# Kernel tuning notes

Hardware: AMD Instinct MI355X
Metric: run time of the kernel (lower is better)

The kernel has to match this reference:

```python
import jax, jax.numpy as jnp
import numpy as np

IMAGE_W, IMAGE_H = 1024, 800
STRIDES = (8, 16, 32, 64, 128)
LEVEL_HW = ((100, 128), (50, 64), (25, 32), (13, 16), (7, 8))
TOP_N = 1000
MIN_SCORE = 0.01
NMS_THR = 0.6
MAX_DET = 100
NUM_CLASSES = 80
BATCH = 16


def _grid(h, w, stride, b):
    ys = (jnp.arange(h, dtype=jnp.float32) + 0.5) * stride
    xs = (jnp.arange(w, dtype=jnp.float32) + 0.5) * stride
    gx, gy = jnp.meshgrid(xs, ys)  # [h, w]
    pos = jnp.stack([gx, gy], axis=-1)  # [h, w, 2] = (x, y)
    return jnp.broadcast_to(pos, (b, h, w, 2))


def setup_inputs() -> dict:
    key = jax.random.key(0)
    inp = {}
    for i, ((h, w), s) in enumerate(zip(LEVEL_HW, STRIDES)):
        key, k1, k2, k3 = jax.random.split(key, 4)
        inp[f"cls{i}"] = jax.random.normal(k1, (BATCH, h, w, NUM_CLASSES), jnp.float32)
        # +3 so exp(reg) gives realistic ~20px box extents
        inp[f"reg{i}"] = jax.random.normal(k2, (BATCH, h, w, 4), jnp.float32) + 3.0
        inp[f"ctr{i}"] = jax.random.normal(k3, (BATCH, h, w, 1), jnp.float32)
        inp[f"pos{i}"] = _grid(h, w, s, BATCH)
    return inp


def _level_filter(cls, reg, ctr, pos):
    b = cls.shape[0]
    cls = jax.nn.sigmoid(cls).reshape(b, -1, NUM_CLASSES)
    reg = jnp.exp(reg).reshape(b, -1, 4)
    ctr = jax.nn.sigmoid(ctr).reshape(b, -1)
    pos = pos.reshape(b, -1, 2)
    scores = jnp.sqrt(jnp.max(cls, axis=2) * ctr)  # [b, n]
    classes = jnp.argmax(cls, axis=2)  # [b, n] int
    if scores.shape[1] >= TOP_N:
        scores, idx = jax.lax.top_k(scores, TOP_N)
        classes = jnp.take_along_axis(classes, idx, axis=1)
        reg = jnp.take_along_axis(reg, idx[..., None], axis=1)
        pos = jnp.take_along_axis(pos, idx[..., None], axis=1)
        cls = jnp.take_along_axis(cls, idx[..., None], axis=1)
    return scores, classes, reg, pos, cls


def _decode_boxes(reg, pos):
    # ltrb offsets -> x1y1x2y2, truncate to int (torch .int()), clamp to image
    xy_min = pos - reg[..., 0:2]
    xy_max = pos + reg[..., 2:4]
    bx = jnp.trunc(jnp.concatenate([xy_min, xy_max], axis=-1))
    x1 = jnp.maximum(bx[..., 0], 0.0)
    y1 = jnp.maximum(bx[..., 1], 0.0)
    x2 = jnp.minimum(bx[..., 2], IMAGE_W - 1.0)
    y2 = jnp.minimum(bx[..., 3], IMAGE_H - 1.0)
    return jnp.stack([x1, y1, x2, y2], axis=-1)


def _nms_image(scores, classes, boxes, clsp):
    valid = scores > MIN_SCORE
    order = jnp.argsort(jnp.where(valid, -scores, jnp.inf))  # valid, desc score first
    s = scores[order]
    c = classes[order].astype(jnp.float32)
    b = boxes[order]
    cp = clsp[order]
    v = valid[order]
    # pairwise IoU (keep/suppress decisions are not differentiated)
    bb = jax.lax.stop_gradient(b)
    area = (bb[:, 2] - bb[:, 0]) * (bb[:, 3] - bb[:, 1])
    lt = jnp.maximum(bb[:, None, :2], bb[None, :, :2])
    rb = jnp.minimum(bb[:, None, 2:], bb[None, :, 2:])
    wh = jnp.maximum(rb - lt, 0.0)
    inter = wh[..., 0] * wh[..., 1]
    iou = inter / (area[:, None] + area[None, :] - inter)
    n = s.shape[0]
    idxs = jnp.arange(n)

    def body(i, keep):
        sup = keep[i] & (iou[i] > NMS_THR) & (idxs > i)
        return keep & ~sup

    keep = jax.lax.fori_loop(0, n, body, v)
    rank = jnp.cumsum(keep) - 1
    slot = jnp.where(keep & (rank < MAX_DET), rank, MAX_DET)  # MAX_DET -> dropped
    out_s = jnp.full((MAX_DET,), -1.0, jnp.float32).at[slot].set(s, mode="drop")
    out_c = jnp.full((MAX_DET,), -1.0, jnp.float32).at[slot].set(c, mode="drop")
    out_b = jnp.full((MAX_DET, 4), -1.0, jnp.float32).at[slot].set(b, mode="drop")
    out_cp = jnp.full((MAX_DET, NUM_CLASSES), -1.0, jnp.float32).at[slot].set(cp, mode="drop")
    return out_s, out_c, out_b, out_cp


def reference(cls0, cls1, cls2, cls3, cls4, reg0, reg1, reg2, reg3, reg4,
              ctr0, ctr1, ctr2, ctr3, ctr4, pos0, pos1, pos2, pos3, pos4):
    clss = [cls0, cls1, cls2, cls3, cls4]
    regs = [reg0, reg1, reg2, reg3, reg4]
    ctrs = [ctr0, ctr1, ctr2, ctr3, ctr4]
    poss = [pos0, pos1, pos2, pos3, pos4]
    parts = [_level_filter(c, r, t, p) for c, r, t, p in zip(clss, regs, ctrs, poss)]
    scores = jnp.concatenate([p[0] for p in parts], axis=1)
    classes = jnp.concatenate([p[1] for p in parts], axis=1)
    reg = jnp.concatenate([p[2] for p in parts], axis=1)
    pos = jnp.concatenate([p[3] for p in parts], axis=1)
    clsp = jnp.concatenate([p[4] for p in parts], axis=1)
    boxes = _decode_boxes(reg, pos)
    return jax.vmap(_nms_image)(scores, classes, boxes, clsp)
```

## Files before the change

kernel.cpp:

```cpp
#include <hip/hip_runtime.h>
#include <math.h>

#define TOTAL_G 17064
#define BATCHN  16
#define ALLF    0xFFFFFFFFFFFFFFFFull
#define INVALID_HI 0xC3DC28F5u

typedef unsigned long long u64;
typedef unsigned int u32;
typedef unsigned short u16;

#define KEYS0_OFF   0
#define KEYS1_OFF   1638400
#define KEYS234_OFF 2048000
#define CLSI_OFF    2187264
#define NC_OFF      2733312
#define T01_OFF     2733568
#define T512_OFF    2733824
#define CK_OFF      2733952
#define K512_OFF    3127168
#define KR_OFF      3192704
#define MSK_OFF     3258240
#define FB_OFF      3782528
#define SLOTK_OFF   4568960

struct Ptrs {
  const float *cls0,*cls1,*cls2,*cls3,*cls4;
  const float *reg0,*reg1,*reg2,*reg3,*reg4;
  const float *ctr0,*ctr1,*ctr2,*ctr3,*ctr4;
  const float *pos0,*pos1,*pos2,*pos3,*pos4;
  char *ws;
};

__device__ __forceinline__ float sigd(float x) {
  return (float)(1.0 / (1.0 + exp(-(double)x)));
}
__device__ __forceinline__ float dexp(float x) {
  return (float)exp((double)x);
}
__device__ __forceinline__ void levinfo(int gid, int& lev, int& idx, int& nl) {
  if      (gid < 12800) { lev=0; idx=gid;        nl=12800; }
  else if (gid < 16000) { lev=1; idx=gid-12800;  nl=3200;  }
  else if (gid < 16800) { lev=2; idx=gid-16000;  nl=800;   }
  else if (gid < 17008) { lev=3; idx=gid-16800;  nl=208;   }
  else                  { lev=4; idx=gid-17008;  nl=56;    }
}

__device__ __forceinline__ u64* ckeys_of(char* ws, int b) {
  return (u64*)(ws + CK_OFF + (size_t)b * 24576);
}
__device__ __forceinline__ u64* key512_of(char* ws, int b) {
  return (u64*)(ws + K512_OFF + (size_t)b * 4096);
}
__device__ __forceinline__ u64* krank_of(char* ws, int b) {
  return (u64*)(ws + KR_OFF + (size_t)b * 4096);
}
__device__ __forceinline__ u64* msk_of(char* ws, int b) {
  return (u64*)(ws + MSK_OFF + (size_t)b * 32768);
}
__device__ __forceinline__ float4* fb_of(char* ws, int b) {
  return (float4*)(ws + FB_OFF + (size_t)b * 49152);
}
__device__ __forceinline__ u64* slotkey_of(char* ws, int b) {
  return (u64*)(ws + SLOTK_OFF + (size_t)b * 800);
}

__device__ __forceinline__ float4 decode_box(const Ptrs& P, int b, int gid) {
  int lev, idx, nl; levinfo(gid, lev, idx, nl);
  const float *rp, *pp;
  if      (lev == 0) { rp = P.reg0; pp = P.pos0; }
  else if (lev == 1) { rp = P.reg1; pp = P.pos1; }
  else if (lev == 2) { rp = P.reg2; pp = P.pos2; }
  else if (lev == 3) { rp = P.reg3; pp = P.pos3; }
  else               { rp = P.reg4; pp = P.pos4; }
  float4 rv = *(const float4*)(rp + (size_t)(b * nl + idx) * 4);
  float2 pv = *(const float2*)(pp + (size_t)(b * nl + idx) * 2);
  float e0 = dexp(rv.x), e1 = dexp(rv.y), e2 = dexp(rv.z), e3 = dexp(rv.w);
  float x1 = truncf(pv.x - e0), y1 = truncf(pv.y - e1);
  float x2 = truncf(pv.x + e2), y2 = truncf(pv.y + e3);
  x1 = fmaxf(x1, 0.0f); y1 = fmaxf(y1, 0.0f);
  x2 = fminf(x2, 1023.0f); y2 = fminf(y2, 799.0f);
  return make_float4(x1, y1, x2, y2);
}

__global__ __launch_bounds__(256) void k_score(Ptrs P) {
  __shared__ float4 sk4[64 * 20];
  int b = blockIdx.y;
  int tid = threadIdx.x;
  int p0 = blockIdx.x * 64;

  #pragma unroll
  for (int it = 0; it < 5; ++it) {
    int t4 = it * 256 + tid;
    int g = p0 + t4 / 20;
    if (g < TOTAL_G) {
      int sub = t4 - (t4 / 20) * 20;
      int lev, idx, nl; levinfo(g, lev, idx, nl);
      const float* clsb;
      if      (lev == 0) clsb = P.cls0;
      else if (lev == 1) clsb = P.cls1;
      else if (lev == 2) clsb = P.cls2;
      else if (lev == 3) clsb = P.cls3;
      else               clsb = P.cls4;
      sk4[t4] = ((const float4*)(clsb + (size_t)(b * nl + idx) * 80))[sub];
    }
  }
  __syncthreads();

  int lp = tid >> 2, q = tid & 3;
  int g = p0 + lp;
  if (g >= TOTAL_G) return;

  const float4* my4 = &sk4[lp * 20 + q * 5];
  float m = -INFINITY, m2 = -INFINITY; int mi = 0;
  #pragma unroll
  for (int k = 0; k < 5; ++k) {
    float4 v = my4[k];
    int base = q * 20 + 4 * k;
    if (v.x > m) { m2 = m; m = v.x; mi = base+0; } else if (v.x > m2) m2 = v.x;
    if (v.y > m) { m2 = m; m = v.y; mi = base+1; } else if (v.y > m2) m2 = v.y;
    if (v.z > m) { m2 = m; m = v.z; mi = base+2; } else if (v.z > m2) m2 = v.z;
    if (v.w > m) { m2 = m; m = v.w; mi = base+3; } else if (v.w > m2) m2 = v.w;
  }
  #pragma unroll
  for (int xw = 1; xw <= 2; xw <<= 1) {
    float om  = __shfl_xor(m,  xw);
    float om2 = __shfl_xor(m2, xw);
    int   omi = __shfl_xor(mi, xw);
    bool take = (om > m) || (om == m && omi < mi);
    float lm  = take ? m : om;
    float wm2 = take ? om2 : m2;
    if (take) { m = om; mi = omi; }
    m2 = fmaxf(lm, wm2);
  }

  float thr = fminf(m - 1e-3f, 9.0f);
  float pmax; int ci;
  if (m2 >= thr) {
    float pv = -1.0f; int pi = 0x7fffffff;
    #pragma unroll 1
    for (int k = 0; k < 5; ++k) {
      float4 v = my4[k];
      float xs[4] = {v.x, v.y, v.z, v.w};
      #pragma unroll
      for (int e = 0; e < 4; ++e) {
        if (xs[e] >= thr) {
          float p = sigd(xs[e]);
          if (p > pv) { pv = p; pi = q * 20 + 4 * k + e; }
        }
      }
    }
    #pragma unroll
    for (int xw = 1; xw <= 2; xw <<= 1) {
      float ov = __shfl_xor(pv, xw);
      int   oi = __shfl_xor(pi, xw);
      if (ov > pv || (ov == pv && oi < pi)) { pv = ov; pi = oi; }
    }
    pmax = pv; ci = pi;
  } else {
    pmax = sigd(m); ci = mi;
  }

  if (q == 0) {
    int lev, idx, nl; levinfo(g, lev, idx, nl);
    const float* ctrb;
    if      (lev == 0) ctrb = P.ctr0;
    else if (lev == 1) ctrb = P.ctr1;
    else if (lev == 2) ctrb = P.ctr2;
    else if (lev == 3) ctrb = P.ctr3;
    else               ctrb = P.ctr4;
    float tc = ctrb[(size_t)b * nl + idx];
    float csig = sigd(tc);
    float prod = pmax * csig;
    float s = (float)sqrt((double)prod);
    ((u16*)(P.ws + CLSI_OFF))[(size_t)b * TOTAL_G + g] = (u16)ci;
    unsigned hi = ~__float_as_uint(s);
    u64 key = ((u64)hi << 15) | (unsigned)g;
    if      (lev == 0) ((u64*)(P.ws + KEYS0_OFF))  [(size_t)b * 12800 + idx] = key;
    else if (lev == 1) ((u64*)(P.ws + KEYS1_OFF))  [(size_t)b * 3200  + idx] = key;
    else               ((u64*)(P.ws + KEYS234_OFF))[(size_t)b * 1088  + (g - 16000)] = key;
  }
}

struct SelSh {
  u32 hist[4][4096];
  u64 buf[64];
  u64 res, pfx;
  int t, mode, cnt;
};

__device__ __forceinline__ u64 loadkey(const Ptrs& P, int b, int u) {
  if (u < 12800) return ((const u64*)(P.ws + KEYS0_OFF))  [(size_t)b * 12800 + u];
  if (u < 16000) return ((const u64*)(P.ws + KEYS1_OFF))  [(size_t)b * 3200  + (u - 12800)];
  return               ((const u64*)(P.ws + KEYS234_OFF))[(size_t)b * 1088  + (u - 16000)];
}
__device__ __forceinline__ bool keep_pred(u64 k, int u, u64 T0, u64 T1) {
  bool valid = (u32)(k >> 15) < INVALID_HI;
  bool sel = (u < 12800) ? (k <= T0) : ((u < 16000) ? (k <= T1) : true);
  return valid && sel;
}

__device__ u64 fast_select(const Ptrs& P, int b, const u64* keys, int n,
                           int pred, int t0, SelSh* S) {
  int tid = threadIdx.x, wid = tid >> 6, lane = tid & 63;
  int rep = wid & 3;
  u64 Pfx = 3; int t = t0;
  const int SS[4] = {33, 21, 9, 0};
  const int WW[4] = {12, 12, 12, 9};
  #pragma unroll 1
  for (int p = 0; p < 4; ++p) {
    int s = SS[p], wb = WW[p];
    u32 dmask = (1u << wb) - 1u;
    for (int i = tid; i < 4 * 4096; i += 1024) (&S->hist[0][0])[i] = 0;
    if (tid == 0) { S->mode = 0; S->cnt = 0; }
    __syncthreads();
    int N = pred ? TOTAL_G : n;
    for (int i = tid; i < N; i += 1024) {
      u64 k = pred ? loadkey(P, b, i) : keys[i];
      if (pred == 2 && !((u32)(k >> 15) < INVALID_HI)) continue;
      if ((k >> (s + wb)) == Pfx)
        atomicAdd(&S->hist[rep][(u32)(k >> s) & dmask], 1u);
    }
    __syncthreads();
    for (int i = tid; i < 4096; i += 1024) {
      u32 v = S->hist[0][i] + S->hist[1][i] + S->hist[2][i] + S->hist[3][i];
      S->hist[0][i] = v;
    }
    __syncthreads();
    if (wid == 0) {
      u32 ssum = 0;
      #pragma unroll 8
      for (int i = 0; i < 64; ++i) {
        int ii = (i + lane) & 63;
        ssum += S->hist[0][(lane << 6) + ii];
      }
      u32 inc = ssum;
      for (int o = 1; o < 64; o <<= 1) { u32 v = __shfl_up(inc, o); if (lane >= o) inc += v; }
      u64 ball = __ballot(inc >= (u32)t);
      if (!ball) {
        if (lane == 0) { S->mode = 9; S->res = ALLF; }
      } else {
        int Wq = __ffsll(ball) - 1;
        u32 cumBefore = __shfl(inc - ssum, Wq);
        u32 v2 = S->hist[0][(Wq << 6) + lane];
        u32 inc2 = v2;
        for (int o = 1; o < 64; o <<= 1) { u32 x = __shfl_up(inc2, o); if (lane >= o) inc2 += x; }
        u64 ball2 = __ballot(cumBefore + inc2 >= (u32)t);
        int l2 = __ffsll(ball2) - 1;
        u32 cumB2 = __shfl(cumBefore + inc2 - v2, l2);
        u32 c = __shfl(v2, l2);
        if (lane == 0) {
          int d = (Wq << 6) + l2;
          u64 np = (Pfx << wb) | (u32)d;
          S->pfx = np; S->t = t - (int)cumB2;
          if (s == 0)       { S->mode = 9; S->res = np; }
          else if (c == 1)  { S->mode = 1; }
          else if (c <= 64) { S->mode = 2; }
        }
      }
    }
    __syncthreads();
    int mode = S->mode; u64 np = S->pfx; int tt = S->t;
    if (mode == 9) return S->res;
    if (mode == 1 || mode == 2) {
      int N2 = pred ? TOTAL_G : n;
      for (int i = tid; i < N2; i += 1024) {
        u64 k = pred ? loadkey(P, b, i) : keys[i];
        if (pred == 2 && !((u32)(k >> 15) < INVALID_HI)) continue;
        if ((k >> s) == np) {
          if (mode == 1) S->res = k;
          else { int pos = atomicAdd(&S->cnt, 1); S->buf[pos] = k; }
        }
      }
      __syncthreads();
      if (mode == 2 && wid == 0) {
        int c2 = S->cnt;
        u64 kl = (lane < c2) ? S->buf[lane] : ALLF;
        int r = 0;
        for (int j = 0; j < c2; ++j) r += (S->buf[j] < kl) ? 1 : 0;
        if (lane < c2 && r == tt - 1) S->res = kl;
      }
      __syncthreads();
      return S->res;
    }
    Pfx = np; t = tt;
    __syncthreads();
  }
  return S->pfx;
}

__global__ __launch_bounds__(1024) void k_sel(Ptrs P) {
  __shared__ SelSh S;
  int b = blockIdx.x, which = blockIdx.y;
  u64 T;
  if (which == 0)
    T = fast_select(P, b, (const u64*)(P.ws + KEYS0_OFF) + (size_t)b * 12800, 12800, 0, 1000, &S);
  else if (which == 1)
    T = fast_select(P, b, (const u64*)(P.ws + KEYS1_OFF) + (size_t)b * 3200, 3200, 0, 1000, &S);
  else
    T = fast_select(P, b, (const u64*)0, 0, 2, 512, &S);
  if (threadIdx.x == 0) {
    if      (which == 0) ((u64*)(P.ws + T01_OFF))[b] = T;
    else if (which == 1) ((u64*)(P.ws + T01_OFF))[16 + b] = T;
    else                 ((u64*)(P.ws + T512_OFF))[b] = T;
  }
}

__global__ __launch_bounds__(1024) void k_comp(Ptrs P) {
  __shared__ int wbase[272], wbase2[272];
  __shared__ int sNc, sN5;
  int b = blockIdx.x;
  int tid = threadIdx.x, wid = tid >> 6, lane = tid & 63;
  u64 T0 = ((u64*)(P.ws + T01_OFF))[b];
  u64 T1 = ((u64*)(P.ws + T01_OFF))[16 + b];
  u64 T512 = ((u64*)(P.ws + T512_OFF))[b];

  for (int it = 0; it < 17; ++it) {
    int u = it * 1024 + tid;
    bool keep = false, keep5 = false;
    if (u < TOTAL_G) {
      u64 k = loadkey(P, b, u);
      keep = keep_pred(k, u, T0, T1);
      keep5 = keep && (k <= T512);
    }
    u64 bal  = __ballot(keep);
    u64 bal5 = __ballot(keep5);
    if (lane == 0) { wbase[it * 16 + wid] = __popcll(bal); wbase2[it * 16 + wid] = __popcll(bal5); }
  }
  __syncthreads();
  if (wid < 2) {
    int* arr = wid ? wbase2 : wbase;
    int carry = 0;
    for (int base = 0; base < 272; base += 64) {
      int idx = base + lane;
      int v = (idx < 272) ? arr[idx] : 0;
      int inc = v;
      for (int o = 1; o < 64; o <<= 1) { int x = __shfl_up(inc, o); if (lane >= o) inc += x; }
      if (idx < 272) arr[idx] = inc - v + carry;
      carry += __shfl(inc, 63);
    }
    if (lane == 0) {
      if (wid) { sN5 = carry; ((int*)(P.ws + NC_OFF))[16 + b] = carry; }
      else     { sNc = carry; ((int*)(P.ws + NC_OFF))[b] = carry; }
    }
  }
  __syncthreads();

  u64* ck  = ckeys_of(P.ws, b);
  u64* k5  = key512_of(P.ws, b);
  for (int it = 0; it < 17; ++it) {
    int u = it * 1024 + tid;
    bool keep = false, keep5 = false; u64 k = 0;
    if (u < TOTAL_G) {
      k = loadkey(P, b, u);
      keep = keep_pred(k, u, T0, T1);
      keep5 = keep && (k <= T512);
    }
    u64 bal  = __ballot(keep);
    u64 bal5 = __ballot(keep5);
    u64 lm = (1ull << lane) - 1ull;
    int pos  = wbase [it * 16 + wid] + __popcll(bal  & lm);
    int pos5 = wbase2[it * 16 + wid] + __popcll(bal5 & lm);
    if (keep)  ck[pos] = k;
    if (keep5) k5[pos5] = k;
  }
}

__global__ __launch_bounds__(1024) void k_mask(Ptrs P) {
  __shared__ u64 skey[512];
  __shared__ float4 sbox[512];
  __shared__ u16 srank[512];
  __shared__ u16 parts[1024];
  __shared__ u64 smaskR[512 * 8];
  int qi = blockIdx.x, b = blockIdx.y;
  int tid = threadIdx.x;
  char* ws = P.ws;
  int n512 = ((int*)(ws + NC_OFF))[16 + b];
  const u64* k5 = key512_of(ws, b);

  if (tid < 512) {
    if (tid < n512) {
      u64 k = k5[tid];
      skey[tid] = k;
      sbox[tid] = decode_box(P, b, (int)(k & 0x7FFF));
    } else {
      skey[tid] = (ALLF - 511) + (u64)tid;
      sbox[tid] = make_float4(-1e30f, -1e30f, -1e30f, -1e30f);
    }
  }
  for (int i = tid; i < 512 * 8; i += 1024) smaskR[i] = 0ull;
  __syncthreads();

  {
    int t2 = tid & 511, half = tid >> 9;
    u64 mykey = skey[t2];
    int jb = half << 8, cnt = 0;
    #pragma unroll 4
    for (int j = jb; j < jb + 256; ++j) cnt += (skey[j] < mykey) ? 1 : 0;
    parts[tid] = (u16)cnt;
  }
  __syncthreads();
  if (tid < 512) srank[tid] = (u16)(parts[tid] + parts[tid + 512]);
  __syncthreads();

  int i = qi * 128 + (tid >> 3);
  int w = tid & 7;
  float4 bi = sbox[i];
  u64 ki = skey[i];
  int ri = srank[i];
  float ia = (bi.z - bi.x) * (bi.w - bi.y);
  #pragma unroll 8
  for (int bj = 0; bj < 64; ++bj) {
    int jj = (bj + w) & 63;
    int j = (w << 6) | jj;
    u64 kj = skey[j];
    if (ki < kj) {
      float4 bj4 = sbox[j];
      float ja  = (bj4.z - bj4.x) * (bj4.w - bj4.y);
      float ltx = fmaxf(bi.x, bj4.x), lty = fmaxf(bi.y, bj4.y);
      float rbx = fminf(bi.z, bj4.z), rby = fminf(bi.w, bj4.w);
      float wv = fmaxf(rbx - ltx, 0.0f), hv = fmaxf(rby - lty, 0.0f);
      float inter = wv * hv;
      float iou = inter / (ia + ja - inter);
      if (iou > 0.6f) {
        int rj = srank[j];
        atomicOr(&smaskR[ri * 8 + (rj >> 6)], 1ull << (rj & 63));
      }
    }
  }
  __syncthreads();

  {
    int il = tid >> 3, ww = tid & 7;
    int ig = qi * 128 + il;
    if (ig < n512) {
      int r = srank[ig];
      msk_of(ws, b)[r * 8 + ww] = smaskR[r * 8 + ww];
      if (ww == 0) krank_of(ws, b)[r] = skey[ig];
    }
  }
}

__global__ __launch_bounds__(256) void k_reduce(Ptrs P) {
  __shared__ u64 smask[4096];
  __shared__ u32 keeplist[100];
  __shared__ int keptS;
  __shared__ u64 liveC[48];
  __shared__ u64 pk[256];
  __shared__ int pc[256];
  __shared__ float4 fkb[100];
  __shared__ u64 bk; __shared__ int bc2;

  int b = blockIdx.x;
  int tid = threadIdx.x;
  char* ws = P.ws;
  int Nc   = ((int*)(ws + NC_OFF))[b];
  int n512 = ((int*)(ws + NC_OFF))[16 + b];
  const u64* ck = ckeys_of(ws, b);
  const u64* kr = krank_of(ws, b);

  const u64* gmask = msk_of(ws, b);
  for (int t = tid; t < 4096; t += 256) smask[t] = gmask[t];
  __syncthreads();

  if (tid < 64) {
    int lane = tid;
    u64 lw = 0;
    if (lane < 8) {
      int lo = lane << 6;
      int c = n512 - lo; if (c < 0) c = 0; if (c > 64) c = 64;
      lw = (c >= 64) ? ALLF : ((c > 0) ? ((1ull << c) - 1ull) : 0ull);
    }
    int kept = 0;
    while (kept < 100) {
      bool nz = (lane < 8) && (lw != 0ull);
      u64 bal = __ballot(nz);
      if (!bal) break;
      int W = __ffsll(bal) - 1;
      u64 wv = __shfl(lw, W);
      int bit = __ffsll(wv) - 1;
      int i = (W << 6) + bit;
      if (lane == 0) keeplist[kept] = (u32)i;
      kept++;
      if (lane == W) lw &= ~(1ull << bit);
      if (kept == 100) break;
      if (lane < 8) lw &= ~smask[i * 8 + lane];
    }
    if (lane == 0) keptS = kept;
  }
  __syncthreads();
  int kept = keptS;

  if (kept < 100 && Nc > 512) {
    u64 T512 = ((u64*)(ws + T512_OFF))[b];
    float4* fb = fb_of(ws, b);
    if (tid < 48) {
      int lo = tid << 6;
      u64 m = 0;
      for (int e = 0; e < 64; ++e) {
        int c = lo + e;
        if (c < Nc && ck[c] > T512) m |= (1ull << e);
      }
      liveC[tid] = m;
    }
    for (int c = tid; c < Nc; c += 256)
      if (ck[c] > T512) fb[c] = decode_box(P, b, (int)(ck[c] & 0x7FFF));
    if (tid < kept) fkb[tid] = decode_box(P, b, (int)(kr[keeplist[tid]] & 0x7FFF));
    __syncthreads();

    for (int k2 = 0; k2 < kept; ++k2) {
      float4 bi = fkb[k2];
      float ia = (bi.z - bi.x) * (bi.w - bi.y);
      for (int j = tid; j < Nc; j += 256) {
        if (!((liveC[j >> 6] >> (j & 63)) & 1ull)) continue;
        float4 bj4 = fb[j];
        float ja  = (bj4.z - bj4.x) * (bj4.w - bj4.y);
        float ltx = fmaxf(bi.x, bj4.x), lty = fmaxf(bi.y, bj4.y);
        float rbx = fminf(bi.z, bj4.z), rby = fminf(bi.w, bj4.w);
        float wv = fmaxf(rbx - ltx, 0.0f), hv = fmaxf(rby - lty, 0.0f);
        float inter = wv * hv;
        float iou = inter / (ia + ja - inter);
        if (iou > 0.6f) atomicAnd(&liveC[j >> 6], ~(1ull << (j & 63)));
      }
    }
    __syncthreads();

    while (kept < 100) {
      u64 mymin = ALLF; int myc = -1;
      for (int c = tid; c < Nc; c += 256) {
        if (!((liveC[c >> 6] >> (c & 63)) & 1ull)) continue;
        u64 k = ck[c];
        if (k < mymin) { mymin = k; myc = c; }
      }
      pk[tid] = mymin; pc[tid] = myc;
      __syncthreads();
      if (tid < 64) {
        u64 m = pk[tid]; int c0 = pc[tid];
        #pragma unroll
        for (int o = 64; o < 256; o += 64)
          if (pk[tid + o] < m) { m = pk[tid + o]; c0 = pc[tid + o]; }
        for (int o = 32; o > 0; o >>= 1) {
          u64 om = __shfl_down(m, o); int oc = __shfl_down(c0, o);
          if (om < m) { m = om; c0 = oc; }
        }
        if (tid == 0) { bk = m; bc2 = c0; }
      }
      __syncthreads();
      if (bk == ALLF) break;
      int cs = bc2;
      if (tid == 0) {
        keeplist[kept] = 0x8000u | (u32)cs;
        atomicAnd(&liveC[cs >> 6], ~(1ull << (cs & 63)));
      }
      __syncthreads();
      kept++;
      if (kept == 100) break;
      float4 bi = fb[cs];
      float ia = (bi.z - bi.x) * (bi.w - bi.y);
      for (int j = tid; j < Nc; j += 256) {
        if (!((liveC[j >> 6] >> (j & 63)) & 1ull)) continue;
        float4 bj4 = fb[j];
        float ja  = (bj4.z - bj4.x) * (bj4.w - bj4.y);
        float ltx = fmaxf(bi.x, bj4.x), lty = fmaxf(bi.y, bj4.y);
        float rbx = fminf(bi.z, bj4.z), rby = fminf(bi.w, bj4.w);
        float wv = fmaxf(rbx - ltx, 0.0f), hv = fmaxf(rby - lty, 0.0f);
        float inter = wv * hv;
        float iou = inter / (ia + ja - inter);
        if (iou > 0.6f) atomicAnd(&liveC[j >> 6], ~(1ull << (j & 63)));
      }
      __syncthreads();
    }
  }

  if (tid < 100) {
    u64 key = ALLF;
    if (tid < kept) {
      u32 e = keeplist[tid];
      key = (e & 0x8000u) ? ck[e & 0x7FFFu] : kr[e];
    }
    slotkey_of(ws, b)[tid] = key;
  }
}

__global__ __launch_bounds__(256) void k_out(Ptrs P, float* out) {
  int b = blockIdx.x, part = blockIdx.y;
  int s0 = part * 10;
  int tid = threadIdx.x;
  const u64* skl = slotkey_of(P.ws, b);

  if (tid < 10) {
    int s = s0 + tid;
    u64 key = skl[s];
    float os = -1.0f, oc = -1.0f;
    float4 bx = make_float4(-1.0f, -1.0f, -1.0f, -1.0f);
    if (key != ALLF) {
      int gid = (int)(key & 0x7FFF);
      os = __uint_as_float(~(u32)(key >> 15));
      oc = (float)((u16*)(P.ws + CLSI_OFF))[(size_t)b * TOTAL_G + gid];
      bx = decode_box(P, b, gid);
    }
    out[b * 100 + s] = os;
    out[1600 + b * 100 + s] = oc;
    *(float4*)(out + 3200 + (size_t)(b * 100 + s) * 4) = bx;
  }

  for (int t = tid; t < 800; t += 256) {
    int sl = t / 80, k = t - sl * 80;
    int s = s0 + sl;
    u64 key = skl[s];
    float val = -1.0f;
    if (key != ALLF) {
      int gid = (int)(key & 0x7FFF);
      int lev, idx, nl; levinfo(gid, lev, idx, nl);
      const float* cp;
      if      (lev == 0) cp = P.cls0;
      else if (lev == 1) cp = P.cls1;
      else if (lev == 2) cp = P.cls2;
      else if (lev == 3) cp = P.cls3;
      else               cp = P.cls4;
      val = sigd(cp[(size_t)(b * nl + idx) * 80 + k]);
    }
    out[9600 + (size_t)(b * 100 + s) * 80 + k] = val;
  }
}

extern "C" void kernel_launch(void* const* d_in, const int* in_sizes, int n_in,
                              void* d_out, int out_size, void* d_ws, size_t ws_size,
                              hipStream_t stream) {
  (void)in_sizes; (void)n_in; (void)out_size; (void)ws_size;
  Ptrs P;
  P.cls0 = (const float*)d_in[0];  P.reg0 = (const float*)d_in[1];
  P.ctr0 = (const float*)d_in[2];  P.pos0 = (const float*)d_in[3];
  P.cls1 = (const float*)d_in[4];  P.reg1 = (const float*)d_in[5];
  P.ctr1 = (const float*)d_in[6];  P.pos1 = (const float*)d_in[7];
  P.cls2 = (const float*)d_in[8];  P.reg2 = (const float*)d_in[9];
  P.ctr2 = (const float*)d_in[10]; P.pos2 = (const float*)d_in[11];
  P.cls3 = (const float*)d_in[12]; P.reg3 = (const float*)d_in[13];
  P.ctr3 = (const float*)d_in[14]; P.pos3 = (const float*)d_in[15];
  P.cls4 = (const float*)d_in[16]; P.reg4 = (const float*)d_in[17];
  P.ctr4 = (const float*)d_in[18]; P.pos4 = (const float*)d_in[19];
  P.ws = (char*)d_ws;

  k_score<<<dim3(267, 16), 256, 0, stream>>>(P);
  k_sel<<<dim3(16, 3), 1024, 0, stream>>>(P);
  k_comp<<<16, 1024, 0, stream>>>(P);
  k_mask<<<dim3(4, 16), 1024, 0, stream>>>(P);
  k_reduce<<<16, 256, 0, stream>>>(P);
  k_out<<<dim3(16, 10), 256, 0, stream>>>(P, (float*)d_out);
}
```

Measured before the change: 114.1 us.

## Fold compaction kernel into mask kernel and drop candidate buffers

Removes the separate k_comp launch. Each k_mask block now recomputes the top-512 compaction into shared memory with a ballot prefix scan. The fallback path in k_reduce no longer uses compacted candidate keys or precomputed boxes; it scans all 17064 anchors with a liveness bitmap and decodes boxes on the fly. This saves one launch and its global writes, but every mask block does redundant full-key scans and the rare fallback path gets much more expensive.

```diff
diff --git a/kernel.cpp b/kernel.cpp
--- a/kernel.cpp
+++ b/kernel.cpp
@@ -17,12 +17,9 @@
 #define NC_OFF      2733312
 #define T01_OFF     2733568
 #define T512_OFF    2733824
-#define CK_OFF      2733952
-#define K512_OFF    3127168
-#define KR_OFF      3192704
-#define MSK_OFF     3258240
-#define FB_OFF      3782528
-#define SLOTK_OFF   4568960
+#define KR_OFF      2733952
+#define MSK_OFF     2799488
+#define SLOTK_OFF   3323776
 
 struct Ptrs {
   const float *cls0,*cls1,*cls2,*cls3,*cls4;
@@ -46,20 +43,11 @@
   else                  { lev=4; idx=gid-17008;  nl=56;    }
 }
 
-__device__ __forceinline__ u64* ckeys_of(char* ws, int b) {
-  return (u64*)(ws + CK_OFF + (size_t)b * 24576);
-}
-__device__ __forceinline__ u64* key512_of(char* ws, int b) {
-  return (u64*)(ws + K512_OFF + (size_t)b * 4096);
-}
 __device__ __forceinline__ u64* krank_of(char* ws, int b) {
   return (u64*)(ws + KR_OFF + (size_t)b * 4096);
 }
 __device__ __forceinline__ u64* msk_of(char* ws, int b) {
   return (u64*)(ws + MSK_OFF + (size_t)b * 32768);
-}
-__device__ __forceinline__ float4* fb_of(char* ws, int b) {
-  return (float4*)(ws + FB_OFF + (size_t)b * 49152);
 }
 __device__ __forceinline__ u64* slotkey_of(char* ws, int b) {
   return (u64*)(ws + SLOTK_OFF + (size_t)b * 800);
@@ -306,89 +294,67 @@
   }
 }
 
-__global__ __launch_bounds__(1024) void k_comp(Ptrs P) {
-  __shared__ int wbase[272], wbase2[272];
-  __shared__ int sNc, sN5;
-  int b = blockIdx.x;
-  int tid = threadIdx.x, wid = tid >> 6, lane = tid & 63;
-  u64 T0 = ((u64*)(P.ws + T01_OFF))[b];
-  u64 T1 = ((u64*)(P.ws + T01_OFF))[16 + b];
-  u64 T512 = ((u64*)(P.ws + T512_OFF))[b];
-
-  for (int it = 0; it < 17; ++it) {
-    int u = it * 1024 + tid;
-    bool keep = false, keep5 = false;
-    if (u < TOTAL_G) {
-      u64 k = loadkey(P, b, u);
-      keep = keep_pred(k, u, T0, T1);
-      keep5 = keep && (k <= T512);
-    }
-    u64 bal  = __ballot(keep);
-    u64 bal5 = __ballot(keep5);
-    if (lane == 0) { wbase[it * 16 + wid] = __popcll(bal); wbase2[it * 16 + wid] = __popcll(bal5); }
-  }
-  __syncthreads();
-  if (wid < 2) {
-    int* arr = wid ? wbase2 : wbase;
-    int carry = 0;
-    for (int base = 0; base < 272; base += 64) {
-      int idx = base + lane;
-      int v = (idx < 272) ? arr[idx] : 0;
-      int inc = v;
-      for (int o = 1; o < 64; o <<= 1) { int x = __shfl_up(inc, o); if (lane >= o) inc += x; }
-      if (idx < 272) arr[idx] = inc - v + carry;
-      carry += __shfl(inc, 63);
-    }
-    if (lane == 0) {
-      if (wid) { sN5 = carry; ((int*)(P.ws + NC_OFF))[16 + b] = carry; }
-      else     { sNc = carry; ((int*)(P.ws + NC_OFF))[b] = carry; }
-    }
-  }
-  __syncthreads();
-
-  u64* ck  = ckeys_of(P.ws, b);
-  u64* k5  = key512_of(P.ws, b);
-  for (int it = 0; it < 17; ++it) {
-    int u = it * 1024 + tid;
-    bool keep = false, keep5 = false; u64 k = 0;
-    if (u < TOTAL_G) {
-      k = loadkey(P, b, u);
-      keep = keep_pred(k, u, T0, T1);
-      keep5 = keep && (k <= T512);
-    }
-    u64 bal  = __ballot(keep);
-    u64 bal5 = __ballot(keep5);
-    u64 lm = (1ull << lane) - 1ull;
-    int pos  = wbase [it * 16 + wid] + __popcll(bal  & lm);
-    int pos5 = wbase2[it * 16 + wid] + __popcll(bal5 & lm);
-    if (keep)  ck[pos] = k;
-    if (keep5) k5[pos5] = k;
-  }
-}
-
 __global__ __launch_bounds__(1024) void k_mask(Ptrs P) {
   __shared__ u64 skey[512];
   __shared__ float4 sbox[512];
   __shared__ u16 srank[512];
   __shared__ u16 parts[1024];
   __shared__ u64 smaskR[512 * 8];
+  __shared__ int wbase[272];
+  __shared__ int sN5;
   int qi = blockIdx.x, b = blockIdx.y;
-  int tid = threadIdx.x;
+  int tid = threadIdx.x, wid = tid >> 6, lane = tid & 63;
   char* ws = P.ws;
-  int n512 = ((int*)(ws + NC_OFF))[16 + b];
-  const u64* k5 = key512_of(ws, b);
-
+  u64 T512 = ((u64*)(ws + T512_OFF))[b];
+
+  for (int it = 0; it < 17; ++it) {
+    int u = it * 1024 + tid;
+    bool keep5 = false;
+    if (u < TOTAL_G) {
+      u64 k = loadkey(P, b, u);
+      keep5 = ((u32)(k >> 15) < INVALID_HI) && (k <= T512);
+    }
+    u64 bal = __ballot(keep5);
+    if (lane == 0) wbase[it * 16 + wid] = __popcll(bal);
+  }
+  for (int i = tid; i < 512 * 8; i += 1024) smaskR[i] = 0ull;
+  __syncthreads();
+  if (wid == 0) {
+    int carry = 0;
+    for (int base = 0; base < 272; base += 64) {
+      int idx = base + lane;
+      int v = (idx < 272) ? wbase[idx] : 0;
+      int inc = v;
+      for (int o = 1; o < 64; o <<= 1) { int x = __shfl_up(inc, o); if (lane >= o) inc += x; }
+      if (idx < 272) wbase[idx] = inc - v + carry;
+      carry += __shfl(inc, 63);
+    }
+    if (lane == 0) sN5 = carry;
+  }
+  __syncthreads();
+  int n512 = sN5;
+  if (qi == 0 && tid == 0) ((int*)(ws + NC_OFF))[16 + b] = n512;
+
+  for (int it = 0; it < 17; ++it) {
+    int u = it * 1024 + tid;
+    bool keep5 = false; u64 k = 0;
+    if (u < TOTAL_G) {
+      k = loadkey(P, b, u);
+      keep5 = ((u32)(k >> 15) < INVALID_HI) && (k <= T512);
+    }
+    u64 bal = __ballot(keep5);
+    int pos = wbase[it * 16 + wid] + __popcll(bal & ((1ull << lane) - 1ull));
+    if (keep5) skey[pos] = k;
+  }
+  __syncthreads();
   if (tid < 512) {
     if (tid < n512) {
-      u64 k = k5[tid];
-      skey[tid] = k;
-      sbox[tid] = decode_box(P, b, (int)(k & 0x7FFF));
+      sbox[tid] = decode_box(P, b, (int)(skey[tid] & 0x7FFF));
     } else {
       skey[tid] = (ALLF - 511) + (u64)tid;
       sbox[tid] = make_float4(-1e30f, -1e30f, -1e30f, -1e30f);
     }
   }
-  for (int i = tid; i < 512 * 8; i += 1024) smaskR[i] = 0ull;
   __syncthreads();
 
   {
@@ -445,7 +411,7 @@
   __shared__ u64 smask[4096];
   __shared__ u32 keeplist[100];
   __shared__ int keptS;
-  __shared__ u64 liveC[48];
+  __shared__ u64 liveC[267];
   __shared__ u64 pk[256];
   __shared__ int pc[256];
   __shared__ float4 fkb[100];
@@ -454,9 +420,7 @@
   int b = blockIdx.x;
   int tid = threadIdx.x;
   char* ws = P.ws;
-  int Nc   = ((int*)(ws + NC_OFF))[b];
   int n512 = ((int*)(ws + NC_OFF))[16 + b];
-  const u64* ck = ckeys_of(ws, b);
   const u64* kr = krank_of(ws, b);
 
   const u64* gmask = msk_of(ws, b);
@@ -490,47 +454,50 @@
   }
   __syncthreads();
   int kept = keptS;
-
-  if (kept < 100 && Nc > 512) {
+  int keptW = kept;
+
+  if (kept < 100 && n512 == 512) {
+    u64 T0   = ((u64*)(ws + T01_OFF))[b];
+    u64 T1   = ((u64*)(ws + T01_OFF))[16 + b];
     u64 T512 = ((u64*)(ws + T512_OFF))[b];
-    float4* fb = fb_of(ws, b);
-    if (tid < 48) {
-      int lo = tid << 6;
+    for (int w = tid; w < 267; w += 256) {
+      int lo = w << 6;
       u64 m = 0;
       for (int e = 0; e < 64; ++e) {
-        int c = lo + e;
-        if (c < Nc && ck[c] > T512) m |= (1ull << e);
-      }
-      liveC[tid] = m;
-    }
-    for (int c = tid; c < Nc; c += 256)
-      if (ck[c] > T512) fb[c] = decode_box(P, b, (int)(ck[c] & 0x7FFF));
+        int u = lo + e;
+        if (u < TOTAL_G) {
+          u64 k = loadkey(P, b, u);
+          if (keep_pred(k, u, T0, T1) && k > T512) m |= (1ull << e);
+        }
+      }
+      liveC[w] = m;
+    }
     if (tid < kept) fkb[tid] = decode_box(P, b, (int)(kr[keeplist[tid]] & 0x7FFF));
     __syncthreads();
 
     for (int k2 = 0; k2 < kept; ++k2) {
       float4 bi = fkb[k2];
       float ia = (bi.z - bi.x) * (bi.w - bi.y);
-      for (int j = tid; j < Nc; j += 256) {
-        if (!((liveC[j >> 6] >> (j & 63)) & 1ull)) continue;
-        float4 bj4 = fb[j];
+      for (int u = tid; u < TOTAL_G; u += 256) {
+        if (!((liveC[u >> 6] >> (u & 63)) & 1ull)) continue;
+        float4 bj4 = decode_box(P, b, u);
         float ja  = (bj4.z - bj4.x) * (bj4.w - bj4.y);
         float ltx = fmaxf(bi.x, bj4.x), lty = fmaxf(bi.y, bj4.y);
         float rbx = fminf(bi.z, bj4.z), rby = fminf(bi.w, bj4.w);
         float wv = fmaxf(rbx - ltx, 0.0f), hv = fmaxf(rby - lty, 0.0f);
         float inter = wv * hv;
         float iou = inter / (ia + ja - inter);
-        if (iou > 0.6f) atomicAnd(&liveC[j >> 6], ~(1ull << (j & 63)));
+        if (iou > 0.6f) atomicAnd(&liveC[u >> 6], ~(1ull << (u & 63)));
       }
     }
     __syncthreads();
 
     while (kept < 100) {
       u64 mymin = ALLF; int myc = -1;
-      for (int c = tid; c < Nc; c += 256) {
-        if (!((liveC[c >> 6] >> (c & 63)) & 1ull)) continue;
-        u64 k = ck[c];
-        if (k < mymin) { mymin = k; myc = c; }
+      for (int u = tid; u < TOTAL_G; u += 256) {
+        if (!((liveC[u >> 6] >> (u & 63)) & 1ull)) continue;
+        u64 k = loadkey(P, b, u);
+        if (k < mymin) { mymin = k; myc = u; }
       }
       pk[tid] = mymin; pc[tid] = myc;
       __syncthreads();
@@ -549,36 +516,32 @@
       if (bk == ALLF) break;
       int cs = bc2;
       if (tid == 0) {
-        keeplist[kept] = 0x8000u | (u32)cs;
+        slotkey_of(ws, b)[kept] = bk;
         atomicAnd(&liveC[cs >> 6], ~(1ull << (cs & 63)));
       }
       __syncthreads();
       kept++;
       if (kept == 100) break;
-      float4 bi = fb[cs];
+      float4 bi = decode_box(P, b, cs);
       float ia = (bi.z - bi.x) * (bi.w - bi.y);
-      for (int j = tid; j < Nc; j += 256) {
-        if (!((liveC[j >> 6] >> (j & 63)) & 1ull)) continue;
-        float4 bj4 = fb[j];
+      for (int u = tid; u < TOTAL_G; u += 256) {
+        if (!((liveC[u >> 6] >> (u & 63)) & 1ull)) continue;
+        float4 bj4 = decode_box(P, b, u);
         float ja  = (bj4.z - bj4.x) * (bj4.w - bj4.y);
         float ltx = fmaxf(bi.x, bj4.x), lty = fmaxf(bi.y, bj4.y);
         float rbx = fminf(bi.z, bj4.z), rby = fminf(bi.w, bj4.w);
         float wv = fmaxf(rbx - ltx, 0.0f), hv = fmaxf(rby - lty, 0.0f);
         float inter = wv * hv;
         float iou = inter / (ia + ja - inter);
-        if (iou > 0.6f) atomicAnd(&liveC[j >> 6], ~(1ull << (j & 63)));
+        if (iou > 0.6f) atomicAnd(&liveC[u >> 6], ~(1ull << (u & 63)));
       }
       __syncthreads();
     }
   }
 
   if (tid < 100) {
-    u64 key = ALLF;
-    if (tid < kept) {
-      u32 e = keeplist[tid];
-      key = (e & 0x8000u) ? ck[e & 0x7FFFu] : kr[e];
-    }
-    slotkey_of(ws, b)[tid] = key;
+    if (tid < keptW)     slotkey_of(ws, b)[tid] = kr[keeplist[tid]];
+    else if (tid >= kept) slotkey_of(ws, b)[tid] = ALLF;
   }
 }
 
@@ -643,7 +606,6 @@
 
   k_score<<<dim3(267, 16), 256, 0, stream>>>(P);
   k_sel<<<dim3(16, 3), 1024, 0, stream>>>(P);
-  k_comp<<<16, 1024, 0, stream>>>(P);
   k_mask<<<dim3(4, 16), 1024, 0, stream>>>(P);
   k_reduce<<<16, 256, 0, stream>>>(P);
   k_out<<<dim3(16, 10), 256, 0, stream>>>(P, (float*)d_out);
```

Result: faster. 111.6 us (-2.2%).
